# Performance work log

Hardware: AMD Instinct MI355X
Metric: run time of the kernel (lower is better)

## Reference

```python
import math
import jax, jax.numpy as jnp
import numpy as np

D_MODEL = 1024
N_HEAD = 16
HEAD_DIM = D_MODEL // N_HEAD  # 64
B = 8
L = 512
USE_GAUSSIAN = True
SCALE = 1.0  # scale=False in __init__


def rel_sin_pos_embed(seq_len, dim):
    # RelativeSinusoidalPositionalEmbedding: table row at index (pos+origin_shift)
    # holds [sin(pos*inv_freq), cos(pos*inv_freq)]; forward selects positions
    # arange(-L/2, round(L/2)) -> for even L this is -L/2 .. L/2-1.
    half = dim // 2
    inv_freq = jnp.exp(jnp.arange(half, dtype=jnp.float32) * (-math.log(10000.0) / (half - 1)))
    rel = jnp.arange(-(seq_len // 2), seq_len - seq_len // 2, dtype=jnp.float32)  # [L]
    ang = rel[:, None] * inv_freq[None, :]  # [L, half]
    return jnp.concatenate([jnp.sin(ang), jnp.cos(ang)], axis=-1)  # [L, dim]


def setup_inputs() -> dict:
    key = jax.random.key(0)
    ks = jax.random.split(key, 8)
    x = jax.random.normal(ks[0], (B, L, D_MODEL), dtype=jnp.float32)
    mask = jax.random.randint(ks[1], (B, L), 0, 2, dtype=jnp.int32)
    # guarantee at least one valid key per row so softmax never sees all -inf
    mask = mask.at[:, 0].set(1)
    qmask = jax.random.randint(ks[2], (B, L), 0, 2, dtype=jnp.int64)
    s = 0.02
    W_qkv = jax.random.normal(ks[3], (5 * D_MODEL, D_MODEL), dtype=jnp.float32) * s
    W_pos = jax.random.normal(ks[4], (3 * D_MODEL, HEAD_DIM), dtype=jnp.float32) * s
    W_fc = jax.random.normal(ks[5], (D_MODEL, D_MODEL), dtype=jnp.float32) * s
    b_fc = jnp.zeros((D_MODEL,), dtype=jnp.float32)
    # shift = abs(randn)+eps (positive), bias = -abs(randn); small scale keeps softmax sane
    shift = jnp.abs(jax.random.normal(ks[6], (1,), dtype=jnp.float32)) * 1e-4 + 1e-5
    bias = -jnp.abs(jax.random.normal(ks[7], (1,), dtype=jnp.float32))
    return {"x": x, "mask": mask, "qmask": qmask, "W_qkv": W_qkv, "W_pos": W_pos,
            "W_fc": W_fc, "b_fc": b_fc, "shift": shift, "bias": bias}


def reference(x, mask, qmask, W_qkv, W_pos, W_fc, b_fc, shift, bias):
    Bs, Ls, D = x.shape
    H, hd = N_HEAD, D // N_HEAD

    qkv = jnp.einsum('bld,ed->ble', x, W_qkv)  # [B, L, 5D]
    q, k, k1, k2, v = jnp.split(qkv, 5, axis=-1)

    def heads(t):  # [B, L, D] -> [B, H, L, hd]
        return t.reshape(Bs, Ls, H, hd).transpose(0, 2, 1, 3)

    q, k1, k2, v = heads(q), heads(k1), heads(k2), heads(v)

    pe = jax.lax.stop_gradient(rel_sin_pos_embed(Ls, hd))  # [L, hd], detached in torch
    y = jnp.einsum('ld,ed->le', pe, W_pos)  # [L, 3D]
    q_p, k1_p, k2_p = jnp.split(y, 3, axis=-1)
    q_p = q_p.reshape(Ls, H, hd).transpose(1, 0, 2)   # [H, L, hd]
    k1_p = k1_p.reshape(Ls, H, hd).transpose(1, 0, 2)  # [H, L, hd]
    k2_p = k2_p.reshape(Ls, H, hd).transpose(1, 0, 2)

    attn_self = jnp.einsum('bhid,bhjd->bhij', q, k1) + jnp.einsum('hid,hjd->hij', q_p, k1_p)[None]
    attn_others = jnp.einsum('bhid,bhjd->bhij', q, k2) + jnp.einsum('hid,hjd->hij', q_p, k2_p)[None]

    same = (qmask[:, :, None] == qmask[:, None, :])[:, None]  # [B, 1, L, L]
    attn = jnp.where(same, attn_self, 0.0) + jnp.where(same, 0.0, attn_others)
    attn = attn / SCALE
    attn = jnp.where(mask[:, None, None, :] == 0, -jnp.inf, attn)

    if USE_GAUSSIAN:
        idx = jnp.arange(Ls, dtype=jnp.float32)
        sq_dist = (idx[:, None] - idx[None, :]) ** 2  # [L, L]
        attn = attn + (-(shift[0] * sq_dist + bias[0]))[None, None]

    attn = jax.nn.softmax(attn, axis=-1)
    out = jnp.einsum('bhij,bhjd->bhid', attn, v)  # [B, H, L, hd]
    out = out.transpose(0, 2, 1, 3).reshape(Bs, Ls, D)
    return jnp.einsum('bld,ed->ble', out, W_fc) + b_fc
```

## Files before the change

kernel.cpp:

```cpp
#include <hip/hip_runtime.h>

#define DM 1024
#define HN 16
#define HD 64
#define BB 8
#define LL 512

typedef __bf16 bf16x8 __attribute__((ext_vector_type(8)));
typedef __bf16 bf16x4 __attribute__((ext_vector_type(4)));
typedef float  f32x4  __attribute__((ext_vector_type(4)));

__device__ __forceinline__ void cvt8(const float* __restrict__ in,
                                     __bf16* __restrict__ out, int i) {
    const float4* p = (const float4*)in + (size_t)i * 2;
    float4 a = p[0], b = p[1];
    bf16x8 v;
    v[0] = (__bf16)a.x; v[1] = (__bf16)a.y; v[2] = (__bf16)a.z; v[3] = (__bf16)a.w;
    v[4] = (__bf16)b.x; v[5] = (__bf16)b.y; v[6] = (__bf16)b.z; v[7] = (__bf16)b.w;
    ((bf16x8*)out)[i] = v;
}

__global__ __launch_bounds__(512) void prep_kernel(
    const int* __restrict__ qmask, const int* __restrict__ maskp,
    const float* __restrict__ x, const float* __restrict__ W_qkv,
    const float* __restrict__ W_pos, const float* __restrict__ W_fc,
    int* __restrict__ perm, int* __restrict__ pmask, float* __restrict__ posf,
    int* __restrict__ nzA, int* __restrict__ sched,
    __bf16* __restrict__ PEb, __bf16* __restrict__ Wposb,
    __bf16* __restrict__ Wfcb, __bf16* __restrict__ Xb, __bf16* __restrict__ Wqkvb)
{
    const int blk = blockIdx.x, tid = threadIdx.x;
    if (blk < 8) {
        int b = blk, i = tid;
        int qm = qmask[b * LL + i];
        unsigned long long bz = __ballot(qm == 0);
        int wid = i >> 6, lane = i & 63;
        __shared__ int wz[8];
        int pzw = __popcll(bz & ((1ULL << lane) - 1ULL));
        if (lane == 0) wz[wid] = __popcll(bz);
        __syncthreads();
        int base = 0, nz = 0;
#pragma unroll
        for (int w2 = 0; w2 < 8; ++w2) { int c = wz[w2]; if (w2 < wid) base += c; nz += c; }
        int zbefore = base + pzw;
        int pos = (qm == 0) ? zbefore : (nz + (i - zbefore));
        perm[b * LL + pos] = i;
        pmask[b * LL + pos] = maskp[b * LL + i];
        posf[b * LL + pos] = (float)i;
        if (i == 0) nzA[b] = nz;
        if (i < 16) {
            int bh2 = b * 16 + i;
            int g = i & 7;
            int idx = b * 2 + (i >> 3);
            int qtm = nz >> 7; if (qtm > 3) qtm = 3;
            sched[idx * 8 + g] = (bh2 << 2) | qtm;
#pragma unroll
            for (int j = 0; j < 3; ++j) {
                int qtj = j + (j >= qtm ? 1 : 0);
                sched[(16 + idx * 3 + j) * 8 + g] = (bh2 << 2) | qtj;
            }
        }
    } else if (blk < 72) {
        int idx = (blk - 8) * 512 + tid;
        int l = idx >> 6, d = idx & 63;
        float p = (float)(l - LL / 2);
        const float cexp = -9.210340371976184f / 31.0f;
        float val;
        if (d < 32) { float f = expf((float)d * cexp);        val = sinf(p * f); }
        else        { float f = expf((float)(d - 32) * cexp); val = cosf(p * f); }
        PEb[idx] = (__bf16)val;
    } else if (blk < 120) {
        cvt8(W_pos, Wposb, (blk - 72) * 512 + tid);
    } else if (blk < 376) {
        cvt8(W_fc, Wfcb, (blk - 120) * 512 + tid);
    } else if (blk < 1400) {
        cvt8(x, Xb, (blk - 376) * 512 + tid);
    } else if (blk < 1656) {
        cvt8(W_qkv, Wqkvb, (blk - 1400) * 512 + tid);
    } else {
        cvt8(W_qkv + 2097152, Wqkvb + 1048576, (blk - 1656) * 512 + tid);
    }
}

__global__ __launch_bounds__(256, 4) void gemm_fused(
    const __bf16* __restrict__ Xb, const __bf16* __restrict__ Wqkvb,
    const __bf16* __restrict__ PEb, const __bf16* __restrict__ Wposb,
    __bf16* __restrict__ Qc, __bf16* __restrict__ K1c,
    __bf16* __restrict__ K2c, __bf16* __restrict__ Vn)
{
    __shared__ __bf16 smem[128 * 136];
    __bf16* As = smem;
    __bf16* Bs = smem + 8192;
    __bf16* Cs = smem;
    const int tid = threadIdx.x;
    const int lane = tid & 63;
    const int w = tid >> 6;
    const int wm = w >> 1, wn = w & 1;

    const bool isPos = (blockIdx.x >= 1024);
    const int bi = isPos ? (blockIdx.x - 1024) : blockIdx.x;
    const int n0 = isPos ? (bi % 24) * 128 : (bi & 31) * 128;
    const int m0 = isPos ? (bi / 24) * 128 : (bi >> 5) * 128;
    const int K  = isPos ? 64 : 1024;
    const __bf16* A  = isPos ? PEb : Xb;
    const __bf16* Bm = isPos ? Wposb : Wqkvb;

    const int fr = lane & 15;
    const int fq = lane >> 4;

    const int srow = tid >> 3;
    const int scol = (tid & 7) ^ (srow & 7);
    const __bf16* Ag = A + (size_t)(m0 + srow) * K + scol * 8;
    const __bf16* Bg = Bm + (size_t)(n0 + srow) * K + scol * 8;
    char* AsB = (char*)As + (size_t)w * 1024;
    char* BsB = (char*)Bs + (size_t)w * 1024;

    f32x4 acc[4][4] = {};

    for (int k0 = 0; k0 < K; k0 += 64) {
#pragma unroll
        for (int r = 0; r < 4; ++r) {
            __builtin_amdgcn_global_load_lds(Ag + k0 + (size_t)(r * 32) * K, AsB + r * 4096, 16, 0, 0);
            __builtin_amdgcn_global_load_lds(Bg + k0 + (size_t)(r * 32) * K, BsB + r * 4096, 16, 0, 0);
        }
        __syncthreads();

#pragma unroll
        for (int kk = 0; kk < 2; ++kk) {
            const int so = ((kk * 4 + fq) ^ (fr & 7)) * 8;
            bf16x8 af[4], bfr[4];
#pragma unroll
            for (int i = 0; i < 4; ++i)
                af[i] = *(const bf16x8*)(As + (size_t)(wm * 64 + i * 16 + fr) * 64 + so);
#pragma unroll
            for (int j = 0; j < 4; ++j)
                bfr[j] = *(const bf16x8*)(Bs + (size_t)(wn * 64 + j * 16 + fr) * 64 + so);
#pragma unroll
            for (int i = 0; i < 4; ++i)
#pragma unroll
                for (int j = 0; j < 4; ++j)
                    acc[i][j] = __builtin_amdgcn_mfma_f32_16x16x32_bf16(bfr[j], af[i], acc[i][j], 0, 0, 0);
        }
        __syncthreads();
    }

#pragma unroll
    for (int i = 0; i < 4; ++i) {
        int mloc = wm * 64 + i * 16 + fr;
#pragma unroll
        for (int j = 0; j < 4; ++j) {
            int nloc = wn * 64 + j * 16 + fq * 4;
            bf16x4 v;
#pragma unroll
            for (int r = 0; r < 4; ++r) v[r] = (__bf16)acc[i][j][r];
            *(bf16x4*)(Cs + (size_t)mloc * 136 + nloc) = v;
        }
    }
    __syncthreads();
    if (!isPos) {
        const int c = n0 >> 10;
        __bf16* T = (c == 0) ? Qc : (c == 1) ? K1c : (c == 2) ? K2c : Vn;
        const int b = m0 >> 9, l0 = m0 & 511, h0 = (n0 >> 6) & 15;
#pragma unroll
        for (int rnd = 0; rnd < 8; ++rnd) {
            int Ci = rnd * 256 + tid;
            int m = Ci >> 4, nch = Ci & 15;
            bf16x8 v = *(const bf16x8*)(Cs + (size_t)m * 136 + nch * 8);
            int hl = nch >> 3, d = (nch & 7) * 8;
            size_t bh2 = (size_t)(b * HN + h0 + hl);
            if (c < 3) *(bf16x8*)(T + (bh2 * LL + l0 + m) * 128 + d) = v;
            else       *(bf16x8*)(T + (bh2 * LL + l0 + m) * 64  + d) = v;
        }
    } else {
        const int c = n0 >> 10;
        __bf16* T = (c == 0) ? Qc : (c == 1) ? K1c : K2c;
#pragma unroll
        for (int rnd = 0; rnd < 8; ++rnd) {
            int Ci = rnd * 256 + tid;
            int m = Ci >> 4, nch = Ci & 15;
            bf16x8 v = *(const bf16x8*)(Cs + (size_t)m * 136 + nch * 8);
            int eg = n0 + nch * 8;
            int h = (eg >> 6) & 15, d = eg & 63;
            size_t off = ((size_t)h * LL + (m0 + m)) * 128 + 64 + d;
#pragma unroll
            for (int b = 0; b < 8; ++b)
                *(bf16x8*)(T + (size_t)b * (HN * LL * 128) + off) = v;
        }
    }
}

__global__ __launch_bounds__(256, 4) void gemm_out(
    const __bf16* __restrict__ A, const __bf16* __restrict__ Bm,
    float* __restrict__ outF, const float* __restrict__ bias)
{
    __shared__ __bf16 smem[128 * 136];
    __bf16* As = smem;
    __bf16* Bs = smem + 8192;
    const int tid = threadIdx.x;
    const int lane = tid & 63;
    const int w = tid >> 6;
    const int wm = w >> 1, wn = w & 1;
    const int n0 = blockIdx.x * 128;
    const int m0 = blockIdx.y * 128;
    const int fr = lane & 15;
    const int fq = lane >> 4;
    const int K = 1024;

    const int srow = tid >> 3;
    const int scol = (tid & 7) ^ (srow & 7);
    const __bf16* Ag = A + (size_t)(m0 + srow) * K + scol * 8;
    const __bf16* Bg = Bm + (size_t)(n0 + srow) * K + scol * 8;
    char* AsB = (char*)As + (size_t)w * 1024;
    char* BsB = (char*)Bs + (size_t)w * 1024;

    f32x4 acc[4][4] = {};

    for (int k0 = 0; k0 < K; k0 += 64) {
#pragma unroll
        for (int r = 0; r < 4; ++r) {
            __builtin_amdgcn_global_load_lds(Ag + k0 + (size_t)(r * 32) * K, AsB + r * 4096, 16, 0, 0);
            __builtin_amdgcn_global_load_lds(Bg + k0 + (size_t)(r * 32) * K, BsB + r * 4096, 16, 0, 0);
        }
        __syncthreads();

#pragma unroll
        for (int kk = 0; kk < 2; ++kk) {
            const int so = ((kk * 4 + fq) ^ (fr & 7)) * 8;
            bf16x8 af[4], bfr[4];
#pragma unroll
            for (int i = 0; i < 4; ++i)
                af[i] = *(const bf16x8*)(As + (size_t)(wm * 64 + i * 16 + fr) * 64 + so);
#pragma unroll
            for (int j = 0; j < 4; ++j)
                bfr[j] = *(const bf16x8*)(Bs + (size_t)(wn * 64 + j * 16 + fr) * 64 + so);
#pragma unroll
            for (int i = 0; i < 4; ++i)
#pragma unroll
                for (int j = 0; j < 4; ++j)
                    acc[i][j] = __builtin_amdgcn_mfma_f32_16x16x32_bf16(bfr[j], af[i], acc[i][j], 0, 0, 0);
        }
        __syncthreads();
    }

#pragma unroll
    for (int i = 0; i < 4; ++i) {
        int m = m0 + wm * 64 + i * 16 + fr;
#pragma unroll
        for (int j = 0; j < 4; ++j) {
            int nn = n0 + wn * 64 + j * 16 + fq * 4;
            float4 bv = *(const float4*)(bias + nn);
            *(float4*)(outF + (size_t)m * DM + nn) =
                make_float4(acc[i][j][0] + bv.x, acc[i][j][1] + bv.y,
                            acc[i][j][2] + bv.z, acc[i][j][3] + bv.w);
        }
    }
}

__global__ __launch_bounds__(256) void vtrans_kernel(const __bf16* __restrict__ Vn,
                                                     const int* __restrict__ perm,
                                                     __bf16* __restrict__ Vt) {
    __shared__ __bf16 Ts[64][72];
    int bh = blockIdx.x >> 3, lt = blockIdx.x & 7;
    int b = bh >> 4;
    int r = threadIdx.x >> 2, s = threadIdx.x & 3;
    int orow = perm[b * LL + lt * 64 + r];
    const __bf16* src = Vn + ((size_t)bh * LL + orow) * 64;
    *(bf16x8*)&Ts[r][s * 16]     = *(const bf16x8*)(src + s * 16);
    *(bf16x8*)&Ts[r][s * 16 + 8] = *(const bf16x8*)(src + s * 16 + 8);
    __syncthreads();
    __bf16* dst = Vt + ((size_t)bh * 64 + r) * LL + lt * 64 + s * 16;
    bf16x8 a, bvv;
#pragma unroll
    for (int e = 0; e < 8; ++e) { a[e] = Ts[s * 16 + e][r]; bvv[e] = Ts[s * 16 + 8 + e][r]; }
    *(bf16x8*)dst = a;
    *(bf16x8*)(dst + 8) = bvv;
}

__global__ __launch_bounds__(512, 2) void attn_kernel(
    const __bf16* __restrict__ Qc, const __bf16* __restrict__ K1c,
    const __bf16* __restrict__ K2c, const __bf16* __restrict__ Vt,
    const int* __restrict__ pmask, const int* __restrict__ perm,
    const float* __restrict__ posf, const int* __restrict__ nzA,
    const int* __restrict__ sched,
    const float* __restrict__ shiftp, __bf16* __restrict__ AO)
{
    __shared__ __bf16 Ke0[64 * 136];
    __shared__ __bf16 Ke1[64 * 136];
    __shared__ __bf16 Vts[64 * 88];
    __shared__ __bf16 Sb[8 * 16 * 72];
    __shared__ __align__(16) float posL[64];

    const int tid = threadIdx.x;
    const int lane = tid & 63;
    const int wid = tid >> 6;
    const int fr = lane & 15;
    const int fq = lane >> 4;

    const int e = sched[blockIdx.x];
    const int qt = e & 3;
    const int h  = (e >> 2) & 15;
    const int b  = e >> 6;
    const size_t bh = (size_t)(b * HN + h);
    const int nz = nzA[b];
    const int q0blk = qt * 128;
    const int s = q0blk + wid * 16 + fr;
    const int pi = perm[b * LL + s];
    const bool need0 = (q0blk < nz);
    const bool need1 = (q0blk + 127 >= nz);
    const int w0 = q0blk + wid * 16;
    const bool wneed0 = (w0 < nz);
    const bool wneed1 = (w0 + 15 >= nz);
    const int qmI = (s >= nz) ? 1 : 0;

    const float sft = shiftp[0];

    bf16x8 qf[4];
    {
        const __bf16* qrow = Qc + (bh * LL + pi) * 128;
#pragma unroll
        for (int kf = 0; kf < 4; ++kf)
            qf[kf] = *(const bf16x8*)(qrow + kf * 32 + fq * 8);
    }

    float mrun = -1e30f, lrun = 0.f;
    f32x4 ot[4] = {};
    const float qposf = (float)pi;

    const __bf16* K1g0 = K1c + bh * LL * 128;
    const __bf16* K2g0 = K2c + bh * LL * 128;
    const __bf16* Vtg0 = Vt + bh * 64 * LL;
    __bf16* Sw = Sb + wid * 16 * 72;

    const int krr = tid >> 4;
    const int ku  = tid & 15;
    const int vrr = tid >> 3;
    const int vu  = tid & 7;

    bf16x8 rk0[2], rk1[2], rv;
    int pm; float ppos;

#define LOAD_TILE(tt)                                                              \
    {                                                                              \
        int j0_ = (tt) * 64;                                                       \
        _Pragma("unroll")                                                          \
        for (int p = 0; p < 2; ++p) {                                              \
            int sr = j0_ + p * 32 + krr;                                           \
            int orow = perm[b * LL + sr];                                          \
            int qmj = (sr >= nz) ? 1 : 0;                                          \
            const __bf16* s1 = (qmj ? K2g0 : K1g0) + (size_t)orow * 128 + ku * 8;  \
            const __bf16* s2 = (qmj ? K1g0 : K2g0) + (size_t)orow * 128 + ku * 8;  \
            if (need0) rk0[p] = *(const bf16x8*)s1;                                \
            if (need1) rk1[p] = *(const bf16x8*)s2;                                \
        }                                                                          \
        rv = *(const bf16x8*)(Vtg0 + (size_t)vrr * LL + j0_ + vu * 8);             \
        pm = pmask[b * LL + j0_ + lane];                                           \
        ppos = posf[b * LL + j0_ + lane];                                          \
    }

    LOAD_TILE(0);

    for (int t = 0; t < 8; ++t) {
        __syncthreads();
        {
#pragma unroll
            for (int p = 0; p < 2; ++p) {
                int rr = p * 32 + krr;
                if (need0) *(bf16x8*)(Ke0 + rr * 136 + ku * 8) = rk0[p];
                if (need1) *(bf16x8*)(Ke1 + rr * 136 + ku * 8) = rk1[p];
            }
            *(bf16x8*)(Vts + vrr * 88 + vu * 8) = rv;
            if (wid == 0) posL[lane] = ppos;
        }
        unsigned long long kbits = __ballot(pm != 0);
        if (t < 7) LOAD_TILE(t + 1);
        __syncthreads();

        f32x4 acc[4];
        if (wneed0 != wneed1) {
            const __bf16* Ks = wneed0 ? Ke0 : Ke1;
            __builtin_amdgcn_s_setprio(1);
#pragma unroll
            for (int kb = 0; kb < 4; ++kb) {
                bf16x8 af[4];
#pragma unroll
                for (int kf = 0; kf < 4; ++kf)
                    af[kf] = *(const bf16x8*)(Ks + (kb * 16 + fr) * 136 + kf * 32 + fq * 8);
                f32x4 a = {};
#pragma unroll
                for (int kf = 0; kf < 4; ++kf)
                    a = __builtin_amdgcn_mfma_f32_16x16x32_bf16(af[kf], qf[kf], a, 0, 0, 0);
                acc[kb] = a;
            }
            __builtin_amdgcn_s_setprio(0);
        } else {
            __builtin_amdgcn_s_setprio(1);
#pragma unroll
            for (int kb = 0; kb < 4; ++kb) {
                bf16x8 a0f[4], a1f[4];
#pragma unroll
                for (int kf = 0; kf < 4; ++kf) {
                    a0f[kf] = *(const bf16x8*)(Ke0 + (kb * 16 + fr) * 136 + kf * 32 + fq * 8);
                    a1f[kf] = *(const bf16x8*)(Ke1 + (kb * 16 + fr) * 136 + kf * 32 + fq * 8);
                }
                f32x4 t0 = {}, t1 = {};
#pragma unroll
                for (int kf = 0; kf < 4; ++kf) {
                    t0 = __builtin_amdgcn_mfma_f32_16x16x32_bf16(a0f[kf], qf[kf], t0, 0, 0, 0);
                    t1 = __builtin_amdgcn_mfma_f32_16x16x32_bf16(a1f[kf], qf[kf], t1, 0, 0, 0);
                }
#pragma unroll
                for (int r = 0; r < 4; ++r) acc[kb][r] = qmI ? t1[r] : t0[r];
            }
            __builtin_amdgcn_s_setprio(0);
        }

#pragma unroll
        for (int kb = 0; kb < 4; ++kb) {
            f32x4 pj = *(const f32x4*)(posL + kb * 16 + fq * 4);
#pragma unroll
            for (int r = 0; r < 4; ++r) {
                float di = qposf - pj[r];
                acc[kb][r] -= sft * di * di;
            }
        }

        float lmax = acc[0][0];
#pragma unroll
        for (int kb = 0; kb < 4; ++kb)
#pragma unroll
            for (int r = 0; r < 4; ++r) lmax = fmaxf(lmax, acc[kb][r]);
        if (!__all(lmax <= mrun + 8.f)) {
            float mn = fmaxf(mrun, lmax);
            mn = fmaxf(mn, __shfl_xor(mn, 16));
            mn = fmaxf(mn, __shfl_xor(mn, 32));
            float sc = __expf(mrun - mn);
            mrun = mn;
            lrun *= sc;
#pragma unroll
            for (int fd = 0; fd < 4; ++fd)
#pragma unroll
                for (int r = 0; r < 4; ++r) ot[fd][r] *= sc;
        }
        float sum = 0.f;
#pragma unroll
        for (int kb = 0; kb < 4; ++kb)
#pragma unroll
            for (int r = 0; r < 4; ++r) {
                int ko = kb * 16 + fq * 4 + r;
                float p = ((int)(kbits >> ko) & 1) ? __expf(acc[kb][r] - mrun) : 0.f;
                acc[kb][r] = p;
                sum += p;
            }
        sum += __shfl_xor(sum, 16);
        sum += __shfl_xor(sum, 32);
        lrun += sum;

#pragma unroll
        for (int kb = 0; kb < 4; ++kb) {
            bf16x4 pk;
#pragma unroll
            for (int r = 0; r < 4; ++r) pk[r] = (__bf16)acc[kb][r];
            *(bf16x4*)(Sw + fr * 72 + kb * 16 + fq * 4) = pk;
        }
        bf16x8 pf0 = *(const bf16x8*)(Sw + fr * 72 + fq * 8);
        bf16x8 pf1 = *(const bf16x8*)(Sw + fr * 72 + 32 + fq * 8);
        __builtin_amdgcn_s_setprio(1);
#pragma unroll
        for (int fd = 0; fd < 4; ++fd) {
            bf16x8 v0 = *(const bf16x8*)(Vts + (fd * 16 + fr) * 88 + fq * 8);
            bf16x8 v1 = *(const bf16x8*)(Vts + (fd * 16 + fr) * 88 + 32 + fq * 8);
            ot[fd] = __builtin_amdgcn_mfma_f32_16x16x32_bf16(v0, pf0, ot[fd], 0, 0, 0);
            ot[fd] = __builtin_amdgcn_mfma_f32_16x16x32_bf16(v1, pf1, ot[fd], 0, 0, 0);
        }
        __builtin_amdgcn_s_setprio(0);
    }
#undef LOAD_TILE

    {
        const float inv = 1.0f / lrun;
#pragma unroll
        for (int fd = 0; fd < 4; ++fd) {
            bf16x4 o;
#pragma unroll
            for (int r = 0; r < 4; ++r) o[r] = (__bf16)(ot[fd][r] * inv);
            *(bf16x4*)(Sw + fr * 72 + fd * 16 + fq * 4) = o;
        }
    }
    __syncthreads();
    {
        int r = tid >> 2, c = tid & 3;
        int pir = perm[b * LL + q0blk + r];
        const __bf16* src = Sb + (r >> 4) * (16 * 72) + (r & 15) * 72;
        __bf16* dst = AO + ((size_t)(b * LL + pir)) * DM + h * 64;
        *(bf16x8*)(dst + c * 8)      = *(const bf16x8*)(src + c * 8);
        *(bf16x8*)(dst + 32 + c * 8) = *(const bf16x8*)(src + 32 + c * 8);
    }
}

extern "C" void kernel_launch(void* const* d_in, const int* in_sizes, int n_in,
                              void* d_out, int out_size, void* d_ws, size_t ws_size,
                              hipStream_t stream) {
    const float* x     = (const float*)d_in[0];
    const int*   mask  = (const int*)d_in[1];
    const int*   qmask = (const int*)d_in[2];
    const float* W_qkv = (const float*)d_in[3];
    const float* W_pos = (const float*)d_in[4];
    const float* W_fc  = (const float*)d_in[5];
    const float* b_fc  = (const float*)d_in[6];
    const float* shift = (const float*)d_in[7];
    const float* bias  = (const float*)d_in[8];
    float* out = (float*)d_out;

    __bf16* Qcb  = (__bf16*)d_ws;
    __bf16* K1cb = Qcb  + 8388608;
    __bf16* K2cb = K1cb + 8388608;
    __bf16* Vnb  = K2cb + 8388608;
    __bf16* Vtb  = Vnb  + 4194304;
    __bf16* Xb   = Vtb  + 4194304;
    __bf16* Wqkvb = Xb  + 4194304;
    __bf16* AOb   = Xb;
    __bf16* PEb   = Wqkvb + 4194304;
    __bf16* Wposb = PEb + 32768;
    __bf16* Wfcb  = Wposb + 196608;
    int* permA = (int*)(Wfcb + 1048576);
    int* nzA   = permA + 4096;
    int* pmaskA = nzA + 8;
    float* posfA = (float*)(pmaskA + 4096);
    int* schedA = (int*)(posfA + 4096);

    prep_kernel<<<2424, 512, 0, stream>>>(qmask, mask, x, W_qkv, W_pos, W_fc,
                                          permA, pmaskA, posfA, nzA, schedA,
                                          PEb, Wposb, Wfcb, Xb, Wqkvb);
    gemm_fused<<<1120, 256, 0, stream>>>(Xb, Wqkvb, PEb, Wposb,
                                         Qcb, K1cb, K2cb, Vnb);
    vtrans_kernel<<<1024, 256, 0, stream>>>(Vnb, permA, Vtb);
    attn_kernel<<<512, 512, 0, stream>>>(Qcb, K1cb, K2cb, Vtb, pmaskA, permA,
                                         posfA, nzA, schedA, shift, AOb);
    gemm_out<<<dim3(8, 32), 256, 0, stream>>>(AOb, Wfcb, out, b_fc);
}
```

Measured before the change: 127.3 us.

## Double-buffer K/V tiles in LDS for single-key-type attention blocks

Adds a specialized path for blocks that need only one of the two key sets (K1 or K2). That path reuses the unused second K buffer as a double buffer, so each iteration needs only one barrier and the next tile is staged while the current one is computed. The P·V product is split into two halves to shrink the per-wave score scratch, and the epilogue stages output through the K buffer instead. Mixed blocks keep the old single-buffered loop, at the cost of more code size and a second code path to keep correct.

```diff
diff --git a/kernel.cpp b/kernel.cpp
--- a/kernel.cpp
+++ b/kernel.cpp
@@ -286,9 +286,9 @@
 {
     __shared__ __bf16 Ke0[64 * 136];
     __shared__ __bf16 Ke1[64 * 136];
-    __shared__ __bf16 Vts[64 * 88];
-    __shared__ __bf16 Sb[8 * 16 * 72];
-    __shared__ __align__(16) float posL[64];
+    __shared__ __bf16 Vts[2][64 * 72];
+    __shared__ __bf16 Sb[8 * 16 * 40];
+    __shared__ __align__(16) float posL[2][64];
 
     const int tid = threadIdx.x;
     const int lane = tid & 63;
@@ -329,17 +329,147 @@
     const __bf16* K1g0 = K1c + bh * LL * 128;
     const __bf16* K2g0 = K2c + bh * LL * 128;
     const __bf16* Vtg0 = Vt + bh * 64 * LL;
-    __bf16* Sw = Sb + wid * 16 * 72;
+    __bf16* Sw = Sb + wid * 16 * 40;
 
     const int krr = tid >> 4;
     const int ku  = tid & 15;
     const int vrr = tid >> 3;
     const int vu  = tid & 7;
 
-    bf16x8 rk0[2], rk1[2], rv;
-    int pm; float ppos;
-
-#define LOAD_TILE(tt)                                                              \
+    if (!(need0 && need1)) {
+        const __bf16* KA = need0 ? K1g0 : K2g0;
+        const __bf16* KB = need0 ? K2g0 : K1g0;
+        bf16x8 rk[2], rv;
+        int pm; float ppos;
+
+#define LOADP(tt)                                                                  \
+    {                                                                              \
+        int j0_ = (tt) * 64;                                                       \
+        _Pragma("unroll")                                                          \
+        for (int p = 0; p < 2; ++p) {                                              \
+            int sr = j0_ + p * 32 + krr;                                           \
+            int orow = perm[b * LL + sr];                                          \
+            rk[p] = *(const bf16x8*)(((sr >= nz) ? KB : KA) + (size_t)orow * 128 + ku * 8); \
+        }                                                                          \
+        rv = *(const bf16x8*)(Vtg0 + (size_t)vrr * LL + j0_ + vu * 8);             \
+        pm = pmask[b * LL + j0_ + lane];                                           \
+        ppos = posf[b * LL + j0_ + lane];                                          \
+    }
+
+#define STAGEP(buf)                                                                \
+    {                                                                              \
+        __bf16* Kd = (buf) ? Ke1 : Ke0;                                            \
+        _Pragma("unroll")                                                          \
+        for (int p = 0; p < 2; ++p) {                                              \
+            int rr = p * 32 + krr;                                                 \
+            *(bf16x8*)(Kd + rr * 136 + ku * 8) = rk[p];                            \
+        }                                                                          \
+        *(bf16x8*)(Vts[buf] + vrr * 72 + vu * 8) = rv;                             \
+        if (wid == 0) posL[buf][lane] = ppos;                                      \
+    }
+
+        LOADP(0);
+        STAGEP(0);
+        unsigned long long kb_next = __ballot(pm != 0);
+        LOADP(1);
+        __syncthreads();
+
+        for (int t = 0; t < 8; ++t) {
+            const int cur = t & 1;
+            const __bf16* Ks = cur ? Ke1 : Ke0;
+            unsigned long long kbits = kb_next;
+
+            f32x4 acc[4];
+            __builtin_amdgcn_s_setprio(1);
+#pragma unroll
+            for (int kb = 0; kb < 4; ++kb) {
+                bf16x8 af[4];
+#pragma unroll
+                for (int kf = 0; kf < 4; ++kf)
+                    af[kf] = *(const bf16x8*)(Ks + (kb * 16 + fr) * 136 + kf * 32 + fq * 8);
+                f32x4 a = {};
+#pragma unroll
+                for (int kf = 0; kf < 4; ++kf)
+                    a = __builtin_amdgcn_mfma_f32_16x16x32_bf16(af[kf], qf[kf], a, 0, 0, 0);
+                acc[kb] = a;
+            }
+            __builtin_amdgcn_s_setprio(0);
+
+#pragma unroll
+            for (int kb = 0; kb < 4; ++kb) {
+                f32x4 pj = *(const f32x4*)(&posL[cur][kb * 16 + fq * 4]);
+#pragma unroll
+                for (int r = 0; r < 4; ++r) {
+                    float di = qposf - pj[r];
+                    acc[kb][r] -= sft * di * di;
+                }
+            }
+
+            float lmax = acc[0][0];
+#pragma unroll
+            for (int kb = 0; kb < 4; ++kb)
+#pragma unroll
+                for (int r = 0; r < 4; ++r) lmax = fmaxf(lmax, acc[kb][r]);
+            if (!__all(lmax <= mrun + 8.f)) {
+                float mn = fmaxf(mrun, lmax);
+                mn = fmaxf(mn, __shfl_xor(mn, 16));
+                mn = fmaxf(mn, __shfl_xor(mn, 32));
+                float sc = __expf(mrun - mn);
+                mrun = mn;
+                lrun *= sc;
+#pragma unroll
+                for (int fd = 0; fd < 4; ++fd)
+#pragma unroll
+                    for (int r = 0; r < 4; ++r) ot[fd][r] *= sc;
+            }
+            float sum = 0.f;
+#pragma unroll
+            for (int kb = 0; kb < 4; ++kb)
+#pragma unroll
+                for (int r = 0; r < 4; ++r) {
+                    int ko = kb * 16 + fq * 4 + r;
+                    float p = ((int)(kbits >> ko) & 1) ? __expf(acc[kb][r] - mrun) : 0.f;
+                    acc[kb][r] = p;
+                    sum += p;
+                }
+            sum += __shfl_xor(sum, 16);
+            sum += __shfl_xor(sum, 32);
+            lrun += sum;
+
+            __builtin_amdgcn_s_setprio(1);
+#pragma unroll
+            for (int half = 0; half < 2; ++half) {
+#pragma unroll
+                for (int kk = 0; kk < 2; ++kk) {
+                    int kb = half * 2 + kk;
+                    bf16x4 pk;
+#pragma unroll
+                    for (int r = 0; r < 4; ++r) pk[r] = (__bf16)acc[kb][r];
+                    *(bf16x4*)(Sw + fr * 40 + kk * 16 + fq * 4) = pk;
+                }
+                bf16x8 pf = *(const bf16x8*)(Sw + fr * 40 + fq * 8);
+#pragma unroll
+                for (int fd = 0; fd < 4; ++fd) {
+                    bf16x8 vf = *(const bf16x8*)(Vts[cur] + (fd * 16 + fr) * 72 + half * 32 + fq * 8);
+                    ot[fd] = __builtin_amdgcn_mfma_f32_16x16x32_bf16(vf, pf, ot[fd], 0, 0, 0);
+                }
+            }
+            __builtin_amdgcn_s_setprio(0);
+
+            if (t < 7) {
+                STAGEP(cur ^ 1);
+                kb_next = __ballot(pm != 0);
+                if (t < 6) LOADP(t + 2);
+                __syncthreads();
+            }
+        }
+#undef LOADP
+#undef STAGEP
+    } else {
+        bf16x8 rk0[2], rk1[2], rv;
+        int pm; float ppos;
+
+#define LOADM(tt)                                                                  \
     {                                                                              \
         int j0_ = (tt) * 64;                                                       \
         _Pragma("unroll")                                                          \
@@ -349,148 +479,151 @@
             int qmj = (sr >= nz) ? 1 : 0;                                          \
             const __bf16* s1 = (qmj ? K2g0 : K1g0) + (size_t)orow * 128 + ku * 8;  \
             const __bf16* s2 = (qmj ? K1g0 : K2g0) + (size_t)orow * 128 + ku * 8;  \
-            if (need0) rk0[p] = *(const bf16x8*)s1;                                \
-            if (need1) rk1[p] = *(const bf16x8*)s2;                                \
+            rk0[p] = *(const bf16x8*)s1;                                           \
+            rk1[p] = *(const bf16x8*)s2;                                           \
         }                                                                          \
         rv = *(const bf16x8*)(Vtg0 + (size_t)vrr * LL + j0_ + vu * 8);             \
         pm = pmask[b * LL + j0_ + lane];                                           \
         ppos = posf[b * LL + j0_ + lane];                                          \
     }
 
-    LOAD_TILE(0);
-
-    for (int t = 0; t < 8; ++t) {
-        __syncthreads();
-        {
-#pragma unroll
-            for (int p = 0; p < 2; ++p) {
-                int rr = p * 32 + krr;
-                if (need0) *(bf16x8*)(Ke0 + rr * 136 + ku * 8) = rk0[p];
-                if (need1) *(bf16x8*)(Ke1 + rr * 136 + ku * 8) = rk1[p];
-            }
-            *(bf16x8*)(Vts + vrr * 88 + vu * 8) = rv;
-            if (wid == 0) posL[lane] = ppos;
-        }
-        unsigned long long kbits = __ballot(pm != 0);
-        if (t < 7) LOAD_TILE(t + 1);
-        __syncthreads();
-
-        f32x4 acc[4];
-        if (wneed0 != wneed1) {
-            const __bf16* Ks = wneed0 ? Ke0 : Ke1;
+        LOADM(0);
+        for (int t = 0; t < 8; ++t) {
+            __syncthreads();
+            {
+#pragma unroll
+                for (int p = 0; p < 2; ++p) {
+                    int rr = p * 32 + krr;
+                    *(bf16x8*)(Ke0 + rr * 136 + ku * 8) = rk0[p];
+                    *(bf16x8*)(Ke1 + rr * 136 + ku * 8) = rk1[p];
+                }
+                *(bf16x8*)(Vts[0] + vrr * 72 + vu * 8) = rv;
+                if (wid == 0) posL[0][lane] = ppos;
+            }
+            unsigned long long kbits = __ballot(pm != 0);
+            if (t < 7) LOADM(t + 1);
+            __syncthreads();
+
+            f32x4 acc[4];
+            if (wneed0 != wneed1) {
+                const __bf16* Ks = wneed0 ? Ke0 : Ke1;
+                __builtin_amdgcn_s_setprio(1);
+#pragma unroll
+                for (int kb = 0; kb < 4; ++kb) {
+                    bf16x8 af[4];
+#pragma unroll
+                    for (int kf = 0; kf < 4; ++kf)
+                        af[kf] = *(const bf16x8*)(Ks + (kb * 16 + fr) * 136 + kf * 32 + fq * 8);
+                    f32x4 a = {};
+#pragma unroll
+                    for (int kf = 0; kf < 4; ++kf)
+                        a = __builtin_amdgcn_mfma_f32_16x16x32_bf16(af[kf], qf[kf], a, 0, 0, 0);
+                    acc[kb] = a;
+                }
+                __builtin_amdgcn_s_setprio(0);
+            } else {
+                __builtin_amdgcn_s_setprio(1);
+#pragma unroll
+                for (int kb = 0; kb < 4; ++kb) {
+                    bf16x8 a0f[4], a1f[4];
+#pragma unroll
+                    for (int kf = 0; kf < 4; ++kf) {
+                        a0f[kf] = *(const bf16x8*)(Ke0 + (kb * 16 + fr) * 136 + kf * 32 + fq * 8);
+                        a1f[kf] = *(const bf16x8*)(Ke1 + (kb * 16 + fr) * 136 + kf * 32 + fq * 8);
+                    }
+                    f32x4 t0 = {}, t1 = {};
+#pragma unroll
+                    for (int kf = 0; kf < 4; ++kf) {
+                        t0 = __builtin_amdgcn_mfma_f32_16x16x32_bf16(a0f[kf], qf[kf], t0, 0, 0, 0);
+                        t1 = __builtin_amdgcn_mfma_f32_16x16x32_bf16(a1f[kf], qf[kf], t1, 0, 0, 0);
+                    }
+#pragma unroll
+                    for (int r = 0; r < 4; ++r) acc[kb][r] = qmI ? t1[r] : t0[r];
+                }
+                __builtin_amdgcn_s_setprio(0);
+            }
+
+#pragma unroll
+            for (int kb = 0; kb < 4; ++kb) {
+                f32x4 pj = *(const f32x4*)(&posL[0][kb * 16 + fq * 4]);
+#pragma unroll
+                for (int r = 0; r < 4; ++r) {
+                    float di = qposf - pj[r];
+                    acc[kb][r] -= sft * di * di;
+                }
+            }
+
+            float lmax = acc[0][0];
+#pragma unroll
+            for (int kb = 0; kb < 4; ++kb)
+#pragma unroll
+                for (int r = 0; r < 4; ++r) lmax = fmaxf(lmax, acc[kb][r]);
+            if (!__all(lmax <= mrun + 8.f)) {
+                float mn = fmaxf(mrun, lmax);
+                mn = fmaxf(mn, __shfl_xor(mn, 16));
+                mn = fmaxf(mn, __shfl_xor(mn, 32));
+                float sc = __expf(mrun - mn);
+                mrun = mn;
+                lrun *= sc;
+#pragma unroll
+                for (int fd = 0; fd < 4; ++fd)
+#pragma unroll
+                    for (int r = 0; r < 4; ++r) ot[fd][r] *= sc;
+            }
+            float sum = 0.f;
+#pragma unroll
+            for (int kb = 0; kb < 4; ++kb)
+#pragma unroll
+                for (int r = 0; r < 4; ++r) {
+                    int ko = kb * 16 + fq * 4 + r;
+                    float p = ((int)(kbits >> ko) & 1) ? __expf(acc[kb][r] - mrun) : 0.f;
+                    acc[kb][r] = p;
+                    sum += p;
+                }
+            sum += __shfl_xor(sum, 16);
+            sum += __shfl_xor(sum, 32);
+            lrun += sum;
+
             __builtin_amdgcn_s_setprio(1);
 #pragma unroll
-            for (int kb = 0; kb < 4; ++kb) {
-                bf16x8 af[4];
-#pragma unroll
-                for (int kf = 0; kf < 4; ++kf)
-                    af[kf] = *(const bf16x8*)(Ks + (kb * 16 + fr) * 136 + kf * 32 + fq * 8);
-                f32x4 a = {};
-#pragma unroll
-                for (int kf = 0; kf < 4; ++kf)
-                    a = __builtin_amdgcn_mfma_f32_16x16x32_bf16(af[kf], qf[kf], a, 0, 0, 0);
-                acc[kb] = a;
+            for (int half = 0; half < 2; ++half) {
+#pragma unroll
+                for (int kk = 0; kk < 2; ++kk) {
+                    int kb = half * 2 + kk;
+                    bf16x4 pk;
+#pragma unroll
+                    for (int r = 0; r < 4; ++r) pk[r] = (__bf16)acc[kb][r];
+                    *(bf16x4*)(Sw + fr * 40 + kk * 16 + fq * 4) = pk;
+                }
+                bf16x8 pf = *(const bf16x8*)(Sw + fr * 40 + fq * 8);
+#pragma unroll
+                for (int fd = 0; fd < 4; ++fd) {
+                    bf16x8 vf = *(const bf16x8*)(Vts[0] + (fd * 16 + fr) * 72 + half * 32 + fq * 8);
+                    ot[fd] = __builtin_amdgcn_mfma_f32_16x16x32_bf16(vf, pf, ot[fd], 0, 0, 0);
+                }
             }
             __builtin_amdgcn_s_setprio(0);
-        } else {
-            __builtin_amdgcn_s_setprio(1);
-#pragma unroll
-            for (int kb = 0; kb < 4; ++kb) {
-                bf16x8 a0f[4], a1f[4];
-#pragma unroll
-                for (int kf = 0; kf < 4; ++kf) {
-                    a0f[kf] = *(const bf16x8*)(Ke0 + (kb * 16 + fr) * 136 + kf * 32 + fq * 8);
-                    a1f[kf] = *(const bf16x8*)(Ke1 + (kb * 16 + fr) * 136 + kf * 32 + fq * 8);
-                }
-                f32x4 t0 = {}, t1 = {};
-#pragma unroll
-                for (int kf = 0; kf < 4; ++kf) {
-                    t0 = __builtin_amdgcn_mfma_f32_16x16x32_bf16(a0f[kf], qf[kf], t0, 0, 0, 0);
-                    t1 = __builtin_amdgcn_mfma_f32_16x16x32_bf16(a1f[kf], qf[kf], t1, 0, 0, 0);
-                }
-#pragma unroll
-                for (int r = 0; r < 4; ++r) acc[kb][r] = qmI ? t1[r] : t0[r];
-            }
-            __builtin_amdgcn_s_setprio(0);
-        }
-
-#pragma unroll
-        for (int kb = 0; kb < 4; ++kb) {
-            f32x4 pj = *(const f32x4*)(posL + kb * 16 + fq * 4);
-#pragma unroll
-            for (int r = 0; r < 4; ++r) {
-                float di = qposf - pj[r];
-                acc[kb][r] -= sft * di * di;
-            }
-        }
-
-        float lmax = acc[0][0];
-#pragma unroll
-        for (int kb = 0; kb < 4; ++kb)
-#pragma unroll
-            for (int r = 0; r < 4; ++r) lmax = fmaxf(lmax, acc[kb][r]);
-        if (!__all(lmax <= mrun + 8.f)) {
-            float mn = fmaxf(mrun, lmax);
-            mn = fmaxf(mn, __shfl_xor(mn, 16));
-            mn = fmaxf(mn, __shfl_xor(mn, 32));
-            float sc = __expf(mrun - mn);
-            mrun = mn;
-            lrun *= sc;
-#pragma unroll
-            for (int fd = 0; fd < 4; ++fd)
-#pragma unroll
-                for (int r = 0; r < 4; ++r) ot[fd][r] *= sc;
-        }
-        float sum = 0.f;
-#pragma unroll
-        for (int kb = 0; kb < 4; ++kb)
-#pragma unroll
-            for (int r = 0; r < 4; ++r) {
-                int ko = kb * 16 + fq * 4 + r;
-                float p = ((int)(kbits >> ko) & 1) ? __expf(acc[kb][r] - mrun) : 0.f;
-                acc[kb][r] = p;
-                sum += p;
-            }
-        sum += __shfl_xor(sum, 16);
-        sum += __shfl_xor(sum, 32);
-        lrun += sum;
-
-#pragma unroll
-        for (int kb = 0; kb < 4; ++kb) {
-            bf16x4 pk;
-#pragma unroll
-            for (int r = 0; r < 4; ++r) pk[r] = (__bf16)acc[kb][r];
-            *(bf16x4*)(Sw + fr * 72 + kb * 16 + fq * 4) = pk;
-        }
-        bf16x8 pf0 = *(const bf16x8*)(Sw + fr * 72 + fq * 8);
-        bf16x8 pf1 = *(const bf16x8*)(Sw + fr * 72 + 32 + fq * 8);
-        __builtin_amdgcn_s_setprio(1);
-#pragma unroll
-        for (int fd = 0; fd < 4; ++fd) {
-            bf16x8 v0 = *(const bf16x8*)(Vts + (fd * 16 + fr) * 88 + fq * 8);
-            bf16x8 v1 = *(const bf16x8*)(Vts + (fd * 16 + fr) * 88 + 32 + fq * 8);
-            ot[fd] = __builtin_amdgcn_mfma_f32_16x16x32_bf16(v0, pf0, ot[fd], 0, 0, 0);
-            ot[fd] = __builtin_amdgcn_mfma_f32_16x16x32_bf16(v1, pf1, ot[fd], 0, 0, 0);
-        }
-        __builtin_amdgcn_s_setprio(0);
-    }
-#undef LOAD_TILE
-
+        }
+#undef LOADM
+    }
+
+    __syncthreads();
     {
         const float inv = 1.0f / lrun;
+        __bf16* Ew = Ke0 + (size_t)(wid * 16) * 72;
 #pragma unroll
         for (int fd = 0; fd < 4; ++fd) {
             bf16x4 o;
 #pragma unroll
             for (int r = 0; r < 4; ++r) o[r] = (__bf16)(ot[fd][r] * inv);
-            *(bf16x4*)(Sw + fr * 72 + fd * 16 + fq * 4) = o;
+            *(bf16x4*)(Ew + fr * 72 + fd * 16 + fq * 4) = o;
         }
     }
     __syncthreads();
     {
         int r = tid >> 2, c = tid & 3;
         int pir = perm[b * LL + q0blk + r];
-        const __bf16* src = Sb + (r >> 4) * (16 * 72) + (r & 15) * 72;
+        const __bf16* src = Ke0 + (size_t)r * 72;
         __bf16* dst = AO + ((size_t)(b * LL + pir)) * DM + h * 64;
         *(bf16x8*)(dst + c * 8)      = *(const bf16x8*)(src + c * 8);
         *(bf16x8*)(dst + 32 + c * 8) = *(const bf16x8*)(src + 32 + c * 8);
```

Measured after the change: 123.0 us (median of 2 runs). -3.4%, faster.
